# Kernel tuning notes

Measured on AMD Instinct MI355X. Metric: run time of the kernel, lower is better.

## Reference

```python
import jax, jax.numpy as jnp
import numpy as np

B = 32; C = 3; IMG = 224; P = 16; G = IMG // P  # 14x14 patches
N = G * G + 1  # 197 tokens incl cls
D = 768; L = 12; H = 12; HD = D // H; FF = 4 * D
NR = (2 * G - 1) * (2 * G - 1) + 3  # 732
SCALE = HD ** -0.5


def _rel_index():
    ch = np.arange(G); cw = np.arange(G)
    coords = np.stack(np.meshgrid(ch, cw, indexing='ij')).reshape(2, -1)
    rel = (coords[:, :, None] - coords[:, None, :]).transpose(1, 2, 0).copy()
    rel[:, :, 0] += G - 1
    rel[:, :, 1] += G - 1
    rel[:, :, 0] *= 2 * G - 1
    idx = np.zeros((N, N), dtype=np.int32)
    idx[1:, 1:] = rel.sum(-1)
    idx[0, :] = NR - 3
    idx[:, 0] = NR - 2
    idx[0, 0] = NR - 1
    return jnp.asarray(idx)


def setup_inputs() -> dict:
    key = jax.random.key(0)
    ks = jax.random.split(key, 10)
    def nrm(k, shape, s=0.02):
        return jax.random.normal(k, shape, jnp.float32) * s
    return {
        'x': jax.random.normal(ks[0], (B, C, IMG, IMG), jnp.float32),
        'patch_w': nrm(ks[1], (D, C, P, P)),
        'patch_b': jnp.zeros((D,), jnp.float32),
        'cls_token': nrm(ks[2], (1, 1, D)),
        'ln1_g': jnp.ones((L, D), jnp.float32), 'ln1_b': jnp.zeros((L, D), jnp.float32),
        'qkv_w': nrm(ks[3], (L, 3 * D, D)),
        'q_bias': jnp.zeros((L, D), jnp.float32), 'v_bias': jnp.zeros((L, D), jnp.float32),
        'rel_table': nrm(ks[4], (L, NR, H)),
        'proj_w': nrm(ks[5], (L, D, D)), 'proj_b': jnp.zeros((L, D), jnp.float32),
        'gamma1': 0.1 * jnp.ones((L, D), jnp.float32),
        'ln2_g': jnp.ones((L, D), jnp.float32), 'ln2_b': jnp.zeros((L, D), jnp.float32),
        'fc1_w': nrm(ks[6], (L, FF, D)), 'fc1_b': jnp.zeros((L, FF), jnp.float32),
        'fc2_w': nrm(ks[7], (L, D, FF)), 'fc2_b': jnp.zeros((L, D), jnp.float32),
        'gamma2': 0.1 * jnp.ones((L, D), jnp.float32),
        'fcn_g': jnp.ones((D,), jnp.float32), 'fcn_b': jnp.zeros((D,), jnp.float32),
        'rel_index': _rel_index(),
    }


def _ln(x, g, b):
    m = x.mean(-1, keepdims=True)
    v = ((x - m) ** 2).mean(-1, keepdims=True)
    return (x - m) * jax.lax.rsqrt(v + 1e-5) * g + b


def reference(x, patch_w, patch_b, cls_token, ln1_g, ln1_b, qkv_w, q_bias, v_bias,
              rel_table, proj_w, proj_b, gamma1, ln2_g, ln2_b, fc1_w, fc1_b,
              fc2_w, fc2_b, gamma2, fcn_g, fcn_b, rel_index):
    b = x.shape[0]
    # patch embed: stride-P conv == unfold + matmul
    xp = x.reshape(b, C, G, P, G, P).transpose(0, 2, 4, 1, 3, 5).reshape(b, G * G, C * P * P)
    tok = xp @ patch_w.reshape(D, C * P * P).T + patch_b  # [B, 196, D]
    tok = jnp.concatenate([jnp.broadcast_to(cls_token, (b, 1, D)), tok], axis=1)  # [B, N, D]

    def block(t, p):
        g1, b1, qw, qb, vb, rt, pw, pb, gm1, g2, b2, f1w, f1b, f2w, f2b, gm2 = p
        h = _ln(t, g1, b1)
        qkv_bias = jnp.concatenate([qb, jnp.zeros_like(qb), vb])
        qkv = (h @ qw.T + qkv_bias).reshape(b, N, 3, H, HD).transpose(2, 0, 3, 1, 4)
        q, k, v = qkv[0] * SCALE, qkv[1], qkv[2]  # [B,H,N,HD]
        rpb = jnp.transpose(rt[rel_index], (2, 0, 1))  # [H,N,N]
        attn = jax.nn.softmax(jnp.einsum('bhid,bhjd->bhij', q, k) + rpb[None], axis=-1)
        o = jnp.einsum('bhij,bhjd->bhid', attn, v).transpose(0, 2, 1, 3).reshape(b, N, D)
        t = t + gm1 * (o @ pw.T + pb)
        h2 = _ln(t, g2, b2)
        m = jax.nn.gelu(h2 @ f1w.T + f1b, approximate=False) @ f2w.T + f2b
        return t + gm2 * m, None

    params = (ln1_g, ln1_b, qkv_w, q_bias, v_bias, rel_table, proj_w, proj_b,
              gamma1, ln2_g, ln2_b, fc1_w, fc1_b, fc2_w, fc2_b, gamma2)
    tok, _ = jax.lax.scan(block, tok, params)
    # BEiT-style mean pooling over patch tokens + fc_norm
    return _ln(tok[:, 1:].mean(axis=1), fcn_g, fcn_b)  # [B, D]
```

## Files before the change

kernel.cpp:

```cpp
#include <hip/hip_runtime.h>


#define BATCH 32
#define NTOK 197
#define NLAYER 12
#define NRR 732
#define MROWS (BATCH * NTOK)
#define MPAD 6400

#define NKV 224
#define QT_N 13
#define VSTR 232
#define PSTR 232
#define RPB_PER_LH (QT_N * 14 * 4 * 16 * 4)
#define RPB_PER_L (RPB_PER_LH * 12)

typedef __attribute__((ext_vector_type(8))) short bf16x8_t;
typedef __attribute__((ext_vector_type(4))) float f32x4_t;

__device__ __forceinline__ unsigned short f2bf_rn(float f) {
  unsigned u = __float_as_uint(f);
  unsigned r = (u + 0x7FFFu + ((u >> 16) & 1u)) >> 16;
  return (unsigned short)r;
}
__device__ __forceinline__ float bf2f(unsigned short u) {
  return __uint_as_float(((unsigned)u) << 16);
}

__device__ __forceinline__ void gld16(const unsigned short* g, unsigned short* l) {
  __builtin_amdgcn_global_load_lds(
      (const __attribute__((address_space(1))) unsigned int*)g,
      (__attribute__((address_space(3))) unsigned int*)l, 16, 0, 0);
}

__global__ void cvt4(const float4* __restrict__ s, ushort4* __restrict__ d, int n4) {
  int i = blockIdx.x * 256 + threadIdx.x;
  if (i >= n4) return;
  float4 v = s[i];
  ushort4 r;
  r.x = f2bf_rn(v.x); r.y = f2bf_rn(v.y); r.z = f2bf_rn(v.z); r.w = f2bf_rn(v.w);
  d[i] = r;
}

__global__ void cvt_layer(const float4* __restrict__ qw, const float4* __restrict__ pw,
                          const float4* __restrict__ f1, const float4* __restrict__ f2,
                          ushort4* __restrict__ dst) {
  const int n_q = 2304 * 768 / 4;
  const int n_p = 768 * 768 / 4;
  const int n_1 = 3072 * 768 / 4;
  int i = blockIdx.x * 256 + threadIdx.x;
  float4 v;
  if (i < n_q) v = qw[i];
  else if (i < n_q + n_p) v = pw[i - n_q];
  else if (i < n_q + n_p + n_1) v = f1[i - n_q - n_p];
  else if (i < n_q + n_p + 2 * n_1) v = f2[i - n_q - n_p - n_1];
  else return;
  ushort4 r;
  r.x = f2bf_rn(v.x); r.y = f2bf_rn(v.y); r.z = f2bf_rn(v.z); r.w = f2bf_rn(v.w);
  dst[i] = r;
}

__global__ void build_rpb(const float* __restrict__ rt, const int* __restrict__ ridx,
                          unsigned short* __restrict__ dst) {
  int idx = blockIdx.x * 256 + threadIdx.x;
  if (idx >= RPB_PER_L * NLAYER) return;
  int r = idx & 3;
  int fr = (idx >> 2) & 15;
  int fq = (idx >> 6) & 3;
  int t2 = idx >> 8;
  int jt = t2 % 14; t2 /= 14;
  int qt = t2 % QT_N; t2 /= QT_N;
  int h = t2 % 12;
  int l = t2 / 12;
  int row = qt * 16 + fq * 4 + r;
  int col = jt * 16 + fr;
  float v = -30000.f;
  if (row < 197 && col < 197)
    v = rt[((size_t)l * NRR + ridx[row * 197 + col]) * 12 + h];
  dst[idx] = f2bf_rn(v);
}

__global__ void build_xp(const float* __restrict__ x, unsigned short* __restrict__ xp) {
  int idx = blockIdx.x * 256 + threadIdx.x;
  if (idx >= 6272 * 768) return;
  int r = idx / 768, c = idx - r * 768;
  int b = r / 196, p = r - b * 196;
  int gy = p / 14, gx = p - gy * 14;
  int ch = c >> 8, rem = c & 255, py = rem >> 4, px = rem & 15;
  float v = x[(((size_t)b * 3 + ch) * 224 + gy * 16 + py) * 224 + gx * 16 + px];
  xp[(size_t)(b * 197 + 1 + p) * 768 + c] = f2bf_rn(v);
}

__global__ void fill_cls(const float* __restrict__ cls, float* __restrict__ tok) {
  int idx = blockIdx.x * 256 + threadIdx.x;
  int b = idx / 768, d = idx - b * 768;
  tok[(size_t)(b * 197) * 768 + d] = cls[d];
}

__global__ __launch_bounds__(256) void ln_rows(const float* __restrict__ x,
                                               unsigned short* __restrict__ y,
                                               const float* __restrict__ g,
                                               const float* __restrict__ b) {
  int row = blockIdx.x;
  const float* xr = x + (size_t)row * 768;
  int t = threadIdx.x;
  float v0 = xr[t], v1 = xr[t + 256], v2 = xr[t + 512];
  float s = v0 + v1 + v2;
  float q = v0 * v0 + v1 * v1 + v2 * v2;
  for (int off = 32; off; off >>= 1) { s += __shfl_xor(s, off); q += __shfl_xor(q, off); }
  __shared__ float rs[4], rq[4];
  int wave = t >> 6;
  if ((t & 63) == 0) { rs[wave] = s; rq[wave] = q; }
  __syncthreads();
  s = rs[0] + rs[1] + rs[2] + rs[3];
  q = rq[0] + rq[1] + rq[2] + rq[3];
  float mean = s * (1.f / 768.f);
  float var = q * (1.f / 768.f) - mean * mean;
  float rstd = rsqrtf(var + 1e-5f);
  unsigned short* yr = y + (size_t)row * 768;
  yr[t]       = f2bf_rn((v0 - mean) * rstd * g[t]       + b[t]);
  yr[t + 256] = f2bf_rn((v1 - mean) * rstd * g[t + 256] + b[t + 256]);
  yr[t + 512] = f2bf_rn((v2 - mean) * rstd * g[t + 512] + b[t + 512]);
}

template <int MODE>
__global__ __launch_bounds__(256, 2) void gemm128(
    const unsigned short* __restrict__ A, const unsigned short* __restrict__ Bw,
    float* __restrict__ Cf, unsigned short* __restrict__ Cb,
    const float* __restrict__ bias, const float* __restrict__ bias2,
    const float* __restrict__ gamma, int K, int N) {
  __shared__ __align__(16) unsigned short As[128 * 32];
  __shared__ __align__(16) unsigned short Bs[128 * 32];
  const int tid = threadIdx.x;
  const int wave = tid >> 6, lane = tid & 63;
  const int m0 = blockIdx.y * 128, n0 = blockIdx.x * 128;
  const int wm = (wave & 1) * 64, wn = (wave >> 1) * 64;
  f32x4_t acc[4][4] = {};
  const int srow = lane >> 2;
  const int scol = (lane & 3) * 8;
  const unsigned short* Abase = A + (size_t)(m0 + srow) * K + scol;
  const unsigned short* Bbase = Bw + (size_t)(n0 + srow) * K + scol;
  const int fr = lane & 15, fq = (lane >> 4) * 8;
  for (int k0 = 0; k0 < K; k0 += 32) {
    __syncthreads();
#pragma unroll
    for (int u0 = 0; u0 < 2; ++u0) {
      int u = wave + u0 * 4;
      gld16(Abase + (size_t)(u * 16) * K + k0, As + u * 512);
      gld16(Bbase + (size_t)(u * 16) * K + k0, Bs + u * 512);
    }
    __syncthreads();
    bf16x8_t af[4], bfr[4];
#pragma unroll
    for (int i = 0; i < 4; ++i) {
      af[i]  = *(const bf16x8_t*)(As + (wm + i * 16 + fr) * 32 + fq);
      bfr[i] = *(const bf16x8_t*)(Bs + (wn + i * 16 + fr) * 32 + fq);
    }
#pragma unroll
    for (int i = 0; i < 4; ++i)
#pragma unroll
      for (int j = 0; j < 4; ++j)
        acc[i][j] = __builtin_amdgcn_mfma_f32_16x16x32_bf16(af[i], bfr[j], acc[i][j], 0, 0, 0);
  }
  const int er = (lane >> 4) * 4;
  const int ec = lane & 15;
#pragma unroll
  for (int i = 0; i < 4; ++i) {
#pragma unroll
    for (int j = 0; j < 4; ++j) {
#pragma unroll
      for (int r = 0; r < 4; ++r) {
        int row = m0 + wm + i * 16 + er + r;
        int col = n0 + wn + j * 16 + ec;
        float v = acc[i][j][r];
        size_t idx = (size_t)row * N + col;
        if constexpr (MODE == 0) {
          Cf[idx] = v + bias[col];
        } else if constexpr (MODE == 1) {
          float bv = (col < 768) ? bias[col] : (col >= 1536 ? bias2[col - 1536] : 0.f);
          v += bv;
          if (col < 768) v *= 0.125f;
          Cb[idx] = f2bf_rn(v);
        } else if constexpr (MODE == 2) {
          Cf[idx] = Cf[idx] + gamma[col] * (v + bias[col]);
        } else {
          float tt = v + bias[col];
          float gv = 0.5f * tt * (1.f + erff(tt * 0.70710678118654752f));
          Cb[idx] = f2bf_rn(gv);
        }
      }
    }
  }
}

__global__ __launch_bounds__(256) void attn_mfma(
    const unsigned short* __restrict__ qkv,
    const unsigned short* __restrict__ rpb,
    unsigned short* __restrict__ o) {
  const int bh = blockIdx.x;
  const int b = bh / 12, h = bh - b * 12;
  __shared__ __align__(16) unsigned short Vt[64 * VSTR];
  __shared__ __align__(16) unsigned short Pls[4][16 * PSTR];
  const int t = threadIdx.x;
  const int wave = t >> 6, lane = t & 63;
  const int fr = lane & 15, fq = lane >> 4;
  const size_t qbase = (size_t)(b * 197) * 2304 + h * 64;
  const unsigned short* rph = rpb + (size_t)h * RPB_PER_LH;

  for (int idx = t; idx < NKV * 16; idx += 256) {
    int j = idx >> 4, d0 = (idx & 15) * 4;
    ushort4 v = *(const ushort4*)(qkv + qbase + 1536 + (size_t)j * 2304 + d0);
    Vt[(d0 + 0) * VSTR + j] = v.x;
    Vt[(d0 + 1) * VSTR + j] = v.y;
    Vt[(d0 + 2) * VSTR + j] = v.z;
    Vt[(d0 + 3) * VSTR + j] = v.w;
  }
  __syncthreads();

  unsigned short* P = &Pls[wave][0];
  for (int qt = wave; qt < QT_N; qt += 4) {
    const unsigned short* qrow = qkv + qbase + (size_t)(qt * 16 + fr) * 2304 + fq * 8;
    bf16x8_t qa0 = *(const bf16x8_t*)(qrow);
    bf16x8_t qa1 = *(const bf16x8_t*)(qrow + 32);
    f32x4_t S[14];
#pragma unroll
    for (int jt = 0; jt < 14; ++jt) {
      const unsigned short* krow = qkv + qbase + 768 + (size_t)(jt * 16 + fr) * 2304 + fq * 8;
      bf16x8_t kb0 = *(const bf16x8_t*)(krow);
      bf16x8_t kb1 = *(const bf16x8_t*)(krow + 32);
      f32x4_t s = {};
      s = __builtin_amdgcn_mfma_f32_16x16x32_bf16(qa0, kb0, s, 0, 0, 0);
      s = __builtin_amdgcn_mfma_f32_16x16x32_bf16(qa1, kb1, s, 0, 0, 0);
      ushort4 rb = *(const ushort4*)(rph + ((size_t)(qt * 14 + jt) * 4 + fq) * 64 + fr * 4);
      s[0] += bf2f(rb.x); s[1] += bf2f(rb.y); s[2] += bf2f(rb.z); s[3] += bf2f(rb.w);
      S[jt] = s;
    }
    float mx[4], sum[4];
#pragma unroll
    for (int r = 0; r < 4; ++r) mx[r] = S[0][r];
#pragma unroll
    for (int jt = 1; jt < 14; ++jt)
#pragma unroll
      for (int r = 0; r < 4; ++r) mx[r] = fmaxf(mx[r], S[jt][r]);
#pragma unroll
    for (int r = 0; r < 4; ++r) {
      for (int off = 1; off < 16; off <<= 1) mx[r] = fmaxf(mx[r], __shfl_xor(mx[r], off));
      sum[r] = 0.f;
    }
#pragma unroll
    for (int jt = 0; jt < 14; ++jt) {
#pragma unroll
      for (int r = 0; r < 4; ++r) {
        float p = __expf(S[jt][r] - mx[r]);
        sum[r] += p;
        P[(fq * 4 + r) * PSTR + jt * 16 + fr] = f2bf_rn(p);
      }
    }
    float rinv[4];
#pragma unroll
    for (int r = 0; r < 4; ++r) {
      for (int off = 1; off < 16; off <<= 1) sum[r] += __shfl_xor(sum[r], off);
      rinv[r] = 1.f / sum[r];
    }
    bf16x8_t pa[7];
#pragma unroll
    for (int ks = 0; ks < 7; ++ks)
      pa[ks] = *(const bf16x8_t*)(P + fr * PSTR + ks * 32 + fq * 8);
#pragma unroll
    for (int nt = 0; nt < 4; ++nt) {
      f32x4_t O = {};
#pragma unroll
      for (int ks = 0; ks < 7; ++ks) {
        bf16x8_t vb = *(const bf16x8_t*)(Vt + (nt * 16 + fr) * VSTR + ks * 32 + fq * 8);
        O = __builtin_amdgcn_mfma_f32_16x16x32_bf16(pa[ks], vb, O, 0, 0, 0);
      }
#pragma unroll
      for (int r = 0; r < 4; ++r) {
        int row = qt * 16 + fq * 4 + r;
        if (row < 197)
          o[(size_t)(b * 197 + row) * 768 + h * 64 + nt * 16 + fr] = f2bf_rn(O[r] * rinv[r]);
      }
    }
  }
}

__global__ __launch_bounds__(256) void pool_ln(const float* __restrict__ tok,
                                               const float* __restrict__ g,
                                               const float* __restrict__ bb,
                                               float* __restrict__ out) {
  int b = blockIdx.x;
  __shared__ float pool[768];
  int t = threadIdx.x;
  for (int c = t; c < 768; c += 256) {
    float s = 0.f;
    const float* p = tok + (size_t)(b * 197 + 1) * 768 + c;
    for (int i = 0; i < 196; ++i) s += p[(size_t)i * 768];
    pool[c] = s * (1.f / 196.f);
  }
  __syncthreads();
  float s = 0.f, q = 0.f;
  for (int c = t; c < 768; c += 256) { float v = pool[c]; s += v; q += v * v; }
  for (int off = 32; off; off >>= 1) { s += __shfl_xor(s, off); q += __shfl_xor(q, off); }
  __shared__ float rs[4], rq[4];
  if ((t & 63) == 0) { rs[t >> 6] = s; rq[t >> 6] = q; }
  __syncthreads();
  s = rs[0] + rs[1] + rs[2] + rs[3];
  q = rq[0] + rq[1] + rq[2] + rq[3];
  float mean = s * (1.f / 768.f);
  float var = q * (1.f / 768.f) - mean * mean;
  float rstd = rsqrtf(var + 1e-5f);
  for (int c = t; c < 768; c += 256)
    out[(size_t)b * 768 + c] = (pool[c] - mean) * rstd * g[c] + bb[c];
}

extern "C" void kernel_launch(void* const* d_in, const int* in_sizes, int n_in,
                              void* d_out, int out_size, void* d_ws, size_t ws_size,
                              hipStream_t stream) {
  const float* x         = (const float*)d_in[0];
  const float* patch_w   = (const float*)d_in[1];
  const float* patch_b   = (const float*)d_in[2];
  const float* cls_tok   = (const float*)d_in[3];
  const float* ln1_g     = (const float*)d_in[4];
  const float* ln1_b     = (const float*)d_in[5];
  const float* qkv_w     = (const float*)d_in[6];
  const float* q_bias    = (const float*)d_in[7];
  const float* v_bias    = (const float*)d_in[8];
  const float* rel_table = (const float*)d_in[9];
  const float* proj_w    = (const float*)d_in[10];
  const float* proj_b    = (const float*)d_in[11];
  const float* gamma1    = (const float*)d_in[12];
  const float* ln2_g     = (const float*)d_in[13];
  const float* ln2_b     = (const float*)d_in[14];
  const float* fc1_w     = (const float*)d_in[15];
  const float* fc1_b     = (const float*)d_in[16];
  const float* fc2_w     = (const float*)d_in[17];
  const float* fc2_b     = (const float*)d_in[18];
  const float* gamma2    = (const float*)d_in[19];
  const float* fcn_g     = (const float*)d_in[20];
  const float* fcn_b     = (const float*)d_in[21];
  const int* rel_index   = (const int*)d_in[22];
  float* out = (float*)d_out;

  char* ws = (char*)d_ws;
  size_t off = 0;
  auto take = [&](size_t bytes) {
    char* p = ws + off;
    off += (bytes + 255) & ~(size_t)255;
    return p;
  };
  unsigned short* wl     = (unsigned short*)take((size_t)8257536 * 2);
  unsigned short* pwb    = (unsigned short*)take((size_t)589824 * 2);
  float*          tokf   = (float*)take((size_t)MPAD * 768 * 4);
  unsigned short* hb     = (unsigned short*)take((size_t)MPAD * 768 * 2);
  unsigned short* qkvb   = (unsigned short*)take((size_t)MPAD * 2304 * 2);
  unsigned short* ffb    = (unsigned short*)take((size_t)MPAD * 3072 * 2);
  unsigned short* rpbAll = (unsigned short*)take((size_t)RPB_PER_L * NLAYER * 2);
  unsigned short* xp = ffb;
  unsigned short* ob = hb;
  unsigned short* wl_qkv = wl;
  unsigned short* wl_proj = wl + (size_t)2304 * 768;
  unsigned short* wl_fc1 = wl_proj + (size_t)768 * 768;
  unsigned short* wl_fc2 = wl_fc1 + (size_t)3072 * 768;

  build_rpb<<<(RPB_PER_L * NLAYER + 255) / 256, 256, 0, stream>>>(rel_table, rel_index, rpbAll);

  cvt4<<<576, 256, 0, stream>>>((const float4*)patch_w, (ushort4*)pwb, 147456);
  build_xp<<<18816, 256, 0, stream>>>(x, xp);
  gemm128<0><<<dim3(6, 50), 256, 0, stream>>>(xp, pwb, tokf, nullptr, patch_b,
                                              nullptr, nullptr, 768, 768);
  fill_cls<<<96, 256, 0, stream>>>(cls_tok, tokf);

  for (int l = 0; l < NLAYER; ++l) {
    cvt_layer<<<6912, 256, 0, stream>>>(
        (const float4*)(qkv_w + (size_t)l * 2304 * 768),
        (const float4*)(proj_w + (size_t)l * 768 * 768),
        (const float4*)(fc1_w + (size_t)l * 3072 * 768),
        (const float4*)(fc2_w + (size_t)l * 768 * 3072), (ushort4*)wl);
    ln_rows<<<MROWS, 256, 0, stream>>>(tokf, hb, ln1_g + l * 768, ln1_b + l * 768);
    gemm128<1><<<dim3(18, 50), 256, 0, stream>>>(hb, wl_qkv, nullptr, qkvb,
                                                 q_bias + l * 768, v_bias + l * 768,
                                                 nullptr, 768, 2304);
    attn_mfma<<<384, 256, 0, stream>>>(qkvb, rpbAll + (size_t)l * RPB_PER_L, ob);
    gemm128<2><<<dim3(6, 50), 256, 0, stream>>>(ob, wl_proj, tokf, nullptr,
                                                proj_b + l * 768, nullptr,
                                                gamma1 + l * 768, 768, 768);
    ln_rows<<<MROWS, 256, 0, stream>>>(tokf, hb, ln2_g + l * 768, ln2_b + l * 768);
    gemm128<3><<<dim3(24, 50), 256, 0, stream>>>(hb, wl_fc1, nullptr, ffb,
                                                 fc1_b + l * 3072, nullptr, nullptr,
                                                 768, 3072);
    gemm128<2><<<dim3(6, 50), 256, 0, stream>>>(ffb, wl_fc2, tokf, nullptr,
                                                fc2_b + l * 768, nullptr,
                                                gamma2 + l * 768, 3072, 768);
  }
  pool_ln<<<32, 256, 0, stream>>>(tokf, fcn_g, fcn_b, out);
}
```

Before: 3.696 ms.

## Templatize GEMM on tile height and split-K, add LDS XOR swizzle

```diff
diff --git a/kernel.cpp b/kernel.cpp
--- a/kernel.cpp
+++ b/kernel.cpp
@@ -14,6 +14,7 @@
 #define PSTR 232
 #define RPB_PER_LH (QT_N * 14 * 4 * 16 * 4)
 #define RPB_PER_L (RPB_PER_LH * 12)
+#define WL_ELEMS 8257536
 
 typedef __attribute__((ext_vector_type(8))) short bf16x8_t;
 typedef __attribute__((ext_vector_type(4))) float f32x4_t;
@@ -123,41 +124,50 @@
   yr[t + 512] = f2bf_rn((v2 - mean) * rstd * g[t + 512] + b[t + 512]);
 }
 
-template <int MODE>
-__global__ __launch_bounds__(256, 2) void gemm128(
+template <int MODE, int BM, int SPLIT>
+__global__ __launch_bounds__(256, 2) void gemm_t(
     const unsigned short* __restrict__ A, const unsigned short* __restrict__ Bw,
     float* __restrict__ Cf, unsigned short* __restrict__ Cb,
     const float* __restrict__ bias, const float* __restrict__ bias2,
     const float* __restrict__ gamma, int K, int N) {
-  __shared__ __align__(16) unsigned short As[128 * 32];
+  constexpr int MI = BM / 32;
+  __shared__ __align__(16) unsigned short As[BM * 32];
   __shared__ __align__(16) unsigned short Bs[128 * 32];
   const int tid = threadIdx.x;
   const int wave = tid >> 6, lane = tid & 63;
-  const int m0 = blockIdx.y * 128, n0 = blockIdx.x * 128;
-  const int wm = (wave & 1) * 64, wn = (wave >> 1) * 64;
-  f32x4_t acc[4][4] = {};
+  const int m0 = blockIdx.y * BM, n0 = blockIdx.x * 128;
+  const int wm = (wave & 1) * (MI * 16), wn = (wave >> 1) * 64;
+  const int KS = K / SPLIT;
+  const int kbase = blockIdx.z * KS;
+  f32x4_t acc[MI][4] = {};
   const int srow = lane >> 2;
-  const int scol = (lane & 3) * 8;
-  const unsigned short* Abase = A + (size_t)(m0 + srow) * K + scol;
-  const unsigned short* Bbase = Bw + (size_t)(n0 + srow) * K + scol;
-  const int fr = lane & 15, fq = (lane >> 4) * 8;
-  for (int k0 = 0; k0 < K; k0 += 32) {
+  const int scol = ((lane & 3) ^ ((lane >> 3) & 3)) * 8;
+  const unsigned short* Abase = A + (size_t)(m0 + srow) * K + kbase + scol;
+  const unsigned short* Bbase = Bw + (size_t)(n0 + srow) * K + kbase + scol;
+  const int fr = lane & 15, fq = lane >> 4;
+  const int rchunk = (fq ^ ((fr >> 1) & 3)) * 8;
+  for (int k0 = 0; k0 < KS; k0 += 32) {
     __syncthreads();
+#pragma unroll
+    for (int u0 = 0; u0 < BM / 64; ++u0) {
+      int u = wave + u0 * 4;
+      gld16(Abase + (size_t)(u * 16) * K + k0, As + u * 512);
+    }
 #pragma unroll
     for (int u0 = 0; u0 < 2; ++u0) {
       int u = wave + u0 * 4;
-      gld16(Abase + (size_t)(u * 16) * K + k0, As + u * 512);
       gld16(Bbase + (size_t)(u * 16) * K + k0, Bs + u * 512);
     }
     __syncthreads();
-    bf16x8_t af[4], bfr[4];
-#pragma unroll
-    for (int i = 0; i < 4; ++i) {
-      af[i]  = *(const bf16x8_t*)(As + (wm + i * 16 + fr) * 32 + fq);
-      bfr[i] = *(const bf16x8_t*)(Bs + (wn + i * 16 + fr) * 32 + fq);
-    }
-#pragma unroll
-    for (int i = 0; i < 4; ++i)
+    bf16x8_t af[MI], bfr[4];
+#pragma unroll
+    for (int i = 0; i < MI; ++i)
+      af[i] = *(const bf16x8_t*)(As + (wm + i * 16 + fr) * 32 + rchunk);
+#pragma unroll
+    for (int j = 0; j < 4; ++j)
+      bfr[j] = *(const bf16x8_t*)(Bs + (wn + j * 16 + fr) * 32 + rchunk);
+#pragma unroll
+    for (int i = 0; i < MI; ++i)
 #pragma unroll
       for (int j = 0; j < 4; ++j)
         acc[i][j] = __builtin_amdgcn_mfma_f32_16x16x32_bf16(af[i], bfr[j], acc[i][j], 0, 0, 0);
@@ -165,7 +175,7 @@
   const int er = (lane >> 4) * 4;
   const int ec = lane & 15;
 #pragma unroll
-  for (int i = 0; i < 4; ++i) {
+  for (int i = 0; i < MI; ++i) {
 #pragma unroll
     for (int j = 0; j < 4; ++j) {
 #pragma unroll
@@ -182,7 +192,12 @@
           if (col < 768) v *= 0.125f;
           Cb[idx] = f2bf_rn(v);
         } else if constexpr (MODE == 2) {
-          Cf[idx] = Cf[idx] + gamma[col] * (v + bias[col]);
+          if constexpr (SPLIT == 1) {
+            Cf[idx] = Cf[idx] + gamma[col] * (v + bias[col]);
+          } else {
+            float add = gamma[col] * (v + (blockIdx.z == 0 ? bias[col] : 0.f));
+            atomicAdd(&Cf[idx], add);
+          }
         } else {
           float tt = v + bias[col];
           float gv = 0.5f * tt * (1.f + erff(tt * 0.70710678118654752f));
@@ -348,7 +363,7 @@
     off += (bytes + 255) & ~(size_t)255;
     return p;
   };
-  unsigned short* wl     = (unsigned short*)take((size_t)8257536 * 2);
+  unsigned short* wl     = (unsigned short*)take((size_t)WL_ELEMS * 2);
   unsigned short* pwb    = (unsigned short*)take((size_t)589824 * 2);
   float*          tokf   = (float*)take((size_t)MPAD * 768 * 4);
   unsigned short* hb     = (unsigned short*)take((size_t)MPAD * 768 * 2);
@@ -366,31 +381,31 @@
 
   cvt4<<<576, 256, 0, stream>>>((const float4*)patch_w, (ushort4*)pwb, 147456);
   build_xp<<<18816, 256, 0, stream>>>(x, xp);
-  gemm128<0><<<dim3(6, 50), 256, 0, stream>>>(xp, pwb, tokf, nullptr, patch_b,
-                                              nullptr, nullptr, 768, 768);
+  gemm_t<0, 64, 1><<<dim3(6, 100), 256, 0, stream>>>(xp, pwb, tokf, nullptr, patch_b,
+                                                     nullptr, nullptr, 768, 768);
   fill_cls<<<96, 256, 0, stream>>>(cls_tok, tokf);
 
   for (int l = 0; l < NLAYER; ++l) {
-    cvt_layer<<<6912, 256, 0, stream>>>(
+    cvt_layer<<<(WL_ELEMS / 4 + 255) / 256, 256, 0, stream>>>(
         (const float4*)(qkv_w + (size_t)l * 2304 * 768),
         (const float4*)(proj_w + (size_t)l * 768 * 768),
         (const float4*)(fc1_w + (size_t)l * 3072 * 768),
         (const float4*)(fc2_w + (size_t)l * 768 * 3072), (ushort4*)wl);
     ln_rows<<<MROWS, 256, 0, stream>>>(tokf, hb, ln1_g + l * 768, ln1_b + l * 768);
-    gemm128<1><<<dim3(18, 50), 256, 0, stream>>>(hb, wl_qkv, nullptr, qkvb,
-                                                 q_bias + l * 768, v_bias + l * 768,
-                                                 nullptr, 768, 2304);
+    gemm_t<1, 128, 1><<<dim3(18, 50), 256, 0, stream>>>(hb, wl_qkv, nullptr, qkvb,
+                                                        q_bias + l * 768, v_bias + l * 768,
+                                                        nullptr, 768, 2304);
     attn_mfma<<<384, 256, 0, stream>>>(qkvb, rpbAll + (size_t)l * RPB_PER_L, ob);
-    gemm128<2><<<dim3(6, 50), 256, 0, stream>>>(ob, wl_proj, tokf, nullptr,
-                                                proj_b + l * 768, nullptr,
-                                                gamma1 + l * 768, 768, 768);
+    gemm_t<2, 64, 1><<<dim3(6, 100), 256, 0, stream>>>(ob, wl_proj, tokf, nullptr,
+                                                       proj_b + l * 768, nullptr,
+                                                       gamma1 + l * 768, 768, 768);
     ln_rows<<<MROWS, 256, 0, stream>>>(tokf, hb, ln2_g + l * 768, ln2_b + l * 768);
-    gemm128<3><<<dim3(24, 50), 256, 0, stream>>>(hb, wl_fc1, nullptr, ffb,
-                                                 fc1_b + l * 3072, nullptr, nullptr,
-                                                 768, 3072);
-    gemm128<2><<<dim3(6, 50), 256, 0, stream>>>(ffb, wl_fc2, tokf, nullptr,
-                                                fc2_b + l * 768, nullptr,
-                                                gamma2 + l * 768, 3072, 768);
+    gemm_t<3, 128, 1><<<dim3(24, 50), 256, 0, stream>>>(hb, wl_fc1, nullptr, ffb,
+                                                        fc1_b + l * 3072, nullptr, nullptr,
+                                                        768, 3072);
+    gemm_t<2, 64, 2><<<dim3(6, 100, 2), 256, 0, stream>>>(ffb, wl_fc2, tokf, nullptr,
+                                                          fc2_b + l * 768, nullptr,
+                                                          gamma2 + l * 768, 3072, 768);
   }
   pool_ln<<<32, 256, 0, stream>>>(tokf, fcn_g, fcn_b, out);
 }
```

Result: faster. 3.494 ms (-5.5%).
